# Optimization experiments

Measured on AMD Instinct MI355X. Metric: run time of the kernel, lower is better.

Reference implementation:

```python
import jax, jax.numpy as jnp
import numpy as np
import math

L, H, NH, DH, E, FF, A, I = 3, 1024, 8, 128, 768, 4096, 100, 50
B, S = 4, 1024
EPS = 1e-5


def _ln(x, g, b):
    m = jnp.mean(x, -1, keepdims=True)
    v = jnp.var(x, -1, keepdims=True)
    return (x - m) * jax.lax.rsqrt(v + EPS) * g + b


def _pos_encoding(seq, d):
    pos = jnp.arange(seq, dtype=jnp.float32)[:, None]
    div = jnp.exp(jnp.arange(0, d, 2, dtype=jnp.float32) * (-math.log(10000.0) / d))
    ang = pos * div  # [S, d/2]
    return jnp.stack([jnp.sin(ang), jnp.cos(ang)], axis=-1).reshape(seq, d)


def setup_inputs() -> dict:
    key = jax.random.key(0)
    ks = jax.random.split(key, 40)
    w = lambda k, s: jax.random.normal(k, s, jnp.float32) * 0.02
    z = lambda s: jnp.zeros(s, jnp.float32)
    d = {}
    d['frame_embeddings'] = jax.random.normal(ks[0], (B, S, E), jnp.float32)
    d['W_in'] = w(ks[1], (H, E)); d['b_in'] = z((H,))
    # _init_weights sets ALL 'weight' params (incl. LayerNorm) to normal(std=0.02)
    d['ln_in_g'] = w(ks[2], (H,)); d['ln_in_b'] = z((H,))
    d['qkv_w'] = w(ks[3], (L, 3 * H, H)); d['qkv_b'] = z((L, 3 * H))
    d['out_w'] = w(ks[4], (L, H, H)); d['out_b'] = z((L, H))
    d['ff1_w'] = w(ks[5], (L, FF, H)); d['ff1_b'] = z((L, FF))
    d['ff2_w'] = w(ks[6], (L, H, FF)); d['ff2_b'] = z((L, H))
    d['n1_g'] = w(ks[7], (L, H)); d['n1_b'] = z((L, H))
    d['n2_g'] = w(ks[8], (L, H)); d['n2_b'] = z((L, H))
    d['ln_out_g'] = w(ks[9], (H,)); d['ln_out_b'] = z((H,))
    d['a1_w'] = w(ks[10], (H, H)); d['a1_b'] = z((H,))
    d['a2_w'] = w(ks[11], (A, H)); d['a2_b'] = z((A,))
    d['i1_w'] = w(ks[12], (H, H)); d['i1_b'] = z((H,))
    d['i2_w'] = w(ks[13], (I, H)); d['i2_b'] = z((I,))
    d['c1_w'] = w(ks[14], (H // 2, H)); d['c1_b'] = z((H // 2,))
    d['c2_w'] = w(ks[15], (1, H // 2)); d['c2_b'] = z((1,))
    d['p_w'] = w(ks[16], (1, H)); d['p_b'] = z((1,))
    d['smoothing_factor'] = jnp.float32(0.7)
    return d


def _encoder_layer(x, qkv_w, qkv_b, out_w, out_b, ff1_w, ff1_b, ff2_w, ff2_b, n1_g, n1_b, n2_g, n2_b):
    # PyTorch post-norm TransformerEncoderLayer (eval: no dropout)
    b, s, _ = x.shape
    qkv = x @ qkv_w.T + qkv_b  # [B,S,3H]
    q, k, v = jnp.split(qkv, 3, axis=-1)
    q = q.reshape(b, s, NH, DH)
    k = k.reshape(b, s, NH, DH)
    v = v.reshape(b, s, NH, DH)
    scores = jnp.einsum('bqhd,bkhd->bhqk', q, k) / math.sqrt(DH)
    attn = jax.nn.softmax(scores, axis=-1)
    ctx = jnp.einsum('bhqk,bkhd->bqhd', attn, v).reshape(b, s, H)
    x = _ln(x + (ctx @ out_w.T + out_b), n1_g, n1_b)
    ff = jax.nn.gelu(x @ ff1_w.T + ff1_b, approximate=False) @ ff2_w.T + ff2_b
    return _ln(x + ff, n2_g, n2_b)


def reference(frame_embeddings, W_in, b_in, ln_in_g, ln_in_b, qkv_w, qkv_b, out_w, out_b,
              ff1_w, ff1_b, ff2_w, ff2_b, n1_g, n1_b, n2_g, n2_b, ln_out_g, ln_out_b,
              a1_w, a1_b, a2_w, a2_b, i1_w, i1_b, i2_w, i2_b, c1_w, c1_b, c2_w, c2_b,
              p_w, p_b, smoothing_factor):
    b, s, _ = frame_embeddings.shape
    h = frame_embeddings @ W_in.T + b_in
    h = h + _pos_encoding(s, H)[None]
    h = _ln(h, ln_in_g, ln_in_b)
    for l in range(L):
        h = _encoder_layer(h, qkv_w[l], qkv_b[l], out_w[l], out_b[l], ff1_w[l], ff1_b[l],
                           ff2_w[l], ff2_b[l], n1_g[l], n1_b[l], n2_g[l], n2_b[l])
    ctx = _ln(h, ln_out_g, ln_out_b)
    action = jax.nn.gelu(ctx @ a1_w.T + a1_b, approximate=False) @ a2_w.T + a2_b  # [B,S,A]
    instr = jax.nn.gelu(ctx @ i1_w.T + i1_b, approximate=False) @ i2_w.T + i2_b  # [B,S,I]
    conf = jax.nn.sigmoid(jax.nn.gelu(ctx @ c1_w.T + c1_b, approximate=False) @ c2_w.T + c2_b)
    # EMA smoothing over time as a single scan (replaces the per-step Python loop)
    sf = jnp.clip(smoothing_factor, 0.0, 1.0)
    both = jnp.concatenate([action, instr], axis=-1)  # [B,S,A+I]
    def step(carry, xt):
        sm = sf * xt + (1.0 - sf) * carry
        return sm, sm
    _, ys = jax.lax.scan(step, both[:, 0], jnp.swapaxes(both[:, 1:], 0, 1))
    smoothed = jnp.concatenate([both[:, :1], jnp.swapaxes(ys, 0, 1)], axis=1)
    action = smoothed[..., :A]
    instr = smoothed[..., A:]
    pool = jax.nn.softmax(ctx @ p_w.T + p_b, axis=1)  # [B,S,1]
    global_ctx = jnp.einsum('bsi,bsh->bih', pool, ctx)[:, 0]  # [B,H]
    return action, instr, conf, pool[..., 0], global_ctx
```

## Files before the change

kernel.cpp:

```cpp
#include <hip/hip_runtime.h>

typedef __attribute__((ext_vector_type(8))) short frag8;
typedef __attribute__((ext_vector_type(4))) float facc4;

#define MFMA16(a,b,c) __builtin_amdgcn_mfma_f32_16x16x32_bf16((a),(b),(c),0,0,0)

__device__ __forceinline__ unsigned short f2bf(float f){
  unsigned int u = __builtin_bit_cast(unsigned int, f);
  u += 0x7FFFu + ((u >> 16) & 1u);
  return (unsigned short)(u >> 16);
}
__device__ __forceinline__ float bf2f(unsigned short h){
  unsigned int u = ((unsigned int)h) << 16;
  return __builtin_bit_cast(float, u);
}
__device__ __forceinline__ float gelu_f(float x){
  return 0.5f * x * (1.0f + erff(x * 0.70710678118654752440f));
}
__device__ __forceinline__ void gload16(const void* g, void* l){
  __builtin_amdgcn_global_load_lds(
      (const __attribute__((address_space(1))) void*)g,
      (__attribute__((address_space(3))) void*)l, 16, 0, 0);
}

struct CvtSeg { const float* src; unsigned short* dst; long total; long blk_start; int rows_src; int K; };
struct CvtArgs { CvtSeg seg[12]; int nseg; };

__global__ void convert_all(CvtArgs a){
  long blk = blockIdx.x;
  int si = 0;
  for (int i = 1; i < a.nseg; i++) if (blk >= a.seg[i].blk_start) si = i;
  CvtSeg s = a.seg[si];
  long i = ((blk - s.blk_start) * 256 + threadIdx.x) * 4L;
  if (i >= s.total) return;
  long row = i / s.K;
  ushort4 o;
  if (row < s.rows_src){
    float4 v = *(const float4*)(s.src + i);
    o.x = f2bf(v.x); o.y = f2bf(v.y); o.z = f2bf(v.z); o.w = f2bf(v.w);
  } else { o.x = 0; o.y = 0; o.z = 0; o.w = 0; }
  *(ushort4*)(s.dst + i) = o;
}

__global__ void pe_kernel(float* __restrict__ pe){
  const int s = blockIdx.x;
  const int t = threadIdx.x;
  float4 o;
#pragma unroll
  for (int e = 0; e < 4; e++){
    int c = t * 4 + e;
    int i2 = c & ~1;
    float dv = expf(-0.0089944730195080f * (float)i2);
    float ang = (float)s * dv;
    ((float*)&o)[e] = (c & 1) ? cosf(ang) : sinf(ang);
  }
  *(float4*)(pe + (size_t)s * 1024 + t * 4) = o;
}

template<int KTOT, int EPI>
__global__ __launch_bounds__(256, 2)
void gemm_p4(const unsigned short* __restrict__ A,
             const unsigned short* __restrict__ W,
             const float* __restrict__ bias,
             void* __restrict__ Cout,
             int ldC, int coloff, int nvalid)
{
  constexpr int BK = 32;
  constexpr int NT = KTOT / BK;
  constexpr int SLOT = 16384;
  static_assert(NT >= 3, "pipeline needs >=3 K-steps");
  __shared__ char lds[4 * SLOT];

  const int tid = threadIdx.x;
  const int w = tid >> 6, lane = tid & 63;
  const int lh = lane & 15, lq = lane >> 4;
  const int wm = w >> 1, wn = w & 1;
  const long row0 = (long)blockIdx.x * 128;
  const long col0 = (long)blockIdx.y * 128;

  facc4 acc[4][4];
  const facc4 vz = {0.f, 0.f, 0.f, 0.f};
#pragma unroll
  for (int r = 0; r < 4; r++)
#pragma unroll
    for (int c = 0; c < 4; c++) acc[r][c] = vz;

  const unsigned short* srcs[4];
#pragma unroll
  for (int i = 0; i < 4; i++){
    const int f = i * 4 + w;
    srcs[i] = (f < 8)
      ? A + (row0 + f * 16 + lh) * (long)KTOT + lq * 8
      : W + (col0 + (f - 8) * 16 + lh) * (long)KTOT + lq * 8;
  }

  auto stage = [&](int slot, int k0){
#pragma unroll
    for (int i = 0; i < 4; i++)
      gload16(srcs[i] + k0, lds + slot * SLOT + (i * 4 + w) * 1024);
  };

  stage(0, 0);
  stage(1, BK);

  for (int t = 0; t < NT; t++){
    if (t + 2 < NT){
      stage((t + 2) & 3, (t + 2) * BK);
      asm volatile("s_waitcnt vmcnt(8)\ns_barrier" ::: "memory");
    } else if (t + 1 < NT){
      asm volatile("s_waitcnt vmcnt(4)\ns_barrier" ::: "memory");
    } else {
      asm volatile("s_waitcnt vmcnt(0)\ns_barrier" ::: "memory");
    }
    __builtin_amdgcn_sched_barrier(0);
    const char* base = lds + (t & 3) * SLOT;
    frag8 af[4], bf[4];
#pragma unroll
    for (int r = 0; r < 4; r++)
      af[r] = *(const frag8*)(base + (wm * 4 + r) * 1024 + lane * 16);
#pragma unroll
    for (int c = 0; c < 4; c++)
      bf[c] = *(const frag8*)(base + 8192 + (wn * 4 + c) * 1024 + lane * 16);
    __builtin_amdgcn_s_setprio(1);
#pragma unroll
    for (int r = 0; r < 4; r++)
#pragma unroll
      for (int c = 0; c < 4; c++)
        acc[r][c] = MFMA16(af[r], bf[c], acc[r][c]);
    __builtin_amdgcn_s_setprio(0);
  }

  if (EPI == 0){
#pragma unroll
    for (int c = 0; c < 4; c++){
      const long gcol = col0 + wn * 64 + c * 16 + lh;
      const bool ok = gcol < nvalid;
      const float bv = ok ? bias[gcol] : 0.f;
#pragma unroll
      for (int r = 0; r < 4; r++){
#pragma unroll
        for (int j = 0; j < 4; j++){
          if (!ok) continue;
          const long grow = row0 + wm * 64 + r * 16 + lq * 4 + j;
          ((float*)Cout)[grow * (long)ldC + coloff + gcol] = acc[r][c][j] + bv;
        }
      }
    }
  } else {
    __syncthreads();
    unsigned short* Es = (unsigned short*)lds;
#pragma unroll
    for (int c = 0; c < 4; c++){
      const int colt = wn * 64 + c * 16 + lh;
      const long gcol = col0 + colt;
      const float bv = (gcol < nvalid) ? bias[gcol] : 0.f;
#pragma unroll
      for (int r = 0; r < 4; r++){
#pragma unroll
        for (int j = 0; j < 4; j++){
          float v = acc[r][c][j] + bv;
          if (EPI == 2) v = gelu_f(v);
          Es[(wm * 64 + r * 16 + lq * 4 + j) * 128 + colt] = f2bf(v);
        }
      }
    }
    __syncthreads();
    unsigned short* outp = (unsigned short*)Cout;
#pragma unroll
    for (int it = 0; it < 8; it++){
      const int row = w * 32 + it * 4 + lq;
      const long grow = row0 + row;
      const long gc0 = col0 + lh * 8;
      const unsigned short* s = &Es[row * 128 + lh * 8];
      if (gc0 + 8 <= nvalid){
        *(uint4*)(outp + grow * (long)ldC + coloff + gc0) = *(const uint4*)s;
      } else {
#pragma unroll
        for (int e = 0; e < 8; e++)
          if (gc0 + e < nvalid) outp[grow * (long)ldC + coloff + gc0 + e] = s[e];
      }
    }
  }
}

__global__ __launch_bounds__(256)
void ln_kernel(const float* __restrict__ a, const float* __restrict__ bsrc, int bmode,
               const float* __restrict__ g, const float* __restrict__ be,
               float* __restrict__ of32, unsigned short* __restrict__ obf)
{
  const int row = blockIdx.x;
  const int t = threadIdx.x;
  float4 x = ((const float4*)(a + (size_t)row * 1024))[t];
  if (bmode){
    const size_t brow = (bmode == 1) ? (size_t)row : (size_t)(row & 1023);
    float4 y = ((const float4*)(bsrc + brow * 1024))[t];
    x.x += y.x; x.y += y.y; x.z += y.z; x.w += y.w;
  }
  float s = x.x + x.y + x.z + x.w;
  float ss = x.x * x.x + x.y * x.y + x.z * x.z + x.w * x.w;
#pragma unroll
  for (int mk = 1; mk < 64; mk <<= 1){ s += __shfl_xor(s, mk); ss += __shfl_xor(ss, mk); }
  __shared__ float red[8];
  const int w = t >> 6, lane = t & 63;
  if (lane == 0){ red[w] = s; red[4 + w] = ss; }
  __syncthreads();
  s = red[0] + red[1] + red[2] + red[3];
  ss = red[4] + red[5] + red[6] + red[7];
  const float mean = s * (1.f / 1024.f);
  const float var = ss * (1.f / 1024.f) - mean * mean;
  const float rstd = rsqrtf(var + 1e-5f);
  float4 gg = ((const float4*)g)[t];
  float4 bb = ((const float4*)be)[t];
  float4 o;
  o.x = (x.x - mean) * rstd * gg.x + bb.x;
  o.y = (x.y - mean) * rstd * gg.y + bb.y;
  o.z = (x.z - mean) * rstd * gg.z + bb.z;
  o.w = (x.w - mean) * rstd * gg.w + bb.w;
  if (of32) ((float4*)(of32 + (size_t)row * 1024))[t] = o;
  if (obf){
    ushort4 hh;
    hh.x = f2bf(o.x); hh.y = f2bf(o.y); hh.z = f2bf(o.z); hh.w = f2bf(o.w);
    ((ushort4*)(obf + (size_t)row * 1024))[t] = hh;
  }
}

__global__ void transpose_v(const unsigned short* __restrict__ qkv, unsigned short* __restrict__ vt){
  __shared__ unsigned short t[32][33];
  const int s0 = blockIdx.x * 32;
  const int d0 = blockIdx.y * 32;
  const int bh = blockIdx.z;
  const int b = bh >> 3, h = bh & 7;
  const int tx = threadIdx.x, ty = threadIdx.y;
#pragma unroll
  for (int j = 0; j < 4; j++){
    int srow = ty + j * 8;
    t[srow][tx] = qkv[(size_t)(b * 1024 + s0 + srow) * 3072 + 2048 + h * 128 + d0 + tx];
  }
  __syncthreads();
#pragma unroll
  for (int j = 0; j < 4; j++){
    int drow = ty + j * 8;
    vt[((size_t)bh * 128 + d0 + drow) * 1024 + s0 + tx] = t[tx][drow];
  }
}

__global__ __launch_bounds__(256, 2)
void attn_kernel(const unsigned short* __restrict__ qkv,
                 const unsigned short* __restrict__ vt,
                 unsigned short* __restrict__ ctx)
{
  const int qt = blockIdx.x, h = blockIdx.y, b = blockIdx.z;
  const int tid = threadIdx.x;
  const int w = tid >> 6, lane = tid & 63;
  const int lh = lane & 15, lq = lane >> 4;

  __shared__ unsigned short Ks[2][64 * 128];
  __shared__ unsigned short Vs[2][128 * 64];
  __shared__ unsigned short P[4][16][72];

  const float scale = 0.08838834764831845f;
  const int q0 = qt * 64 + w * 16;

  frag8 qf[4];
#pragma unroll
  for (int kk = 0; kk < 4; kk++)
    qf[kk] = *(const frag8*)(qkv + ((size_t)(b * 1024 + q0 + lh)) * 3072 + h * 128 + kk * 32 + lq * 8);

  const unsigned short* Kg = qkv + (size_t)b * 1024 * 3072 + 1024 + h * 128;
  const unsigned short* Vg = vt + (size_t)(b * 8 + h) * 128 * 1024;

  const int k_rsub = lane >> 4;
  const int k_c    = lane & 15;
  const int v_rsub = lane >> 3;
  const int v_c    = lane & 7;

  auto stage = [&](int buf, int kv0){
#pragma unroll
    for (int i = 0; i < 4; i++){
      const int seg = i * 4 + w;
      const int kr = seg * 4 + k_rsub;
      const int ksc = k_c ^ (kr & 7);
      gload16(Kg + (size_t)(kv0 + kr) * 3072 + ksc * 8,
              (char*)Ks + buf * 16384 + seg * 1024);
      const int vr = seg * 8 + v_rsub;
      const int vsc = v_c ^ (vr & 7);
      gload16(Vg + (size_t)vr * 1024 + kv0 + vsc * 8,
              (char*)Vs + buf * 16384 + seg * 1024);
    }
  };

  facc4 O[8];
  const facc4 vz = {0.f, 0.f, 0.f, 0.f};
#pragma unroll
  for (int c = 0; c < 8; c++) O[c] = vz;
  float m[4], l[4];
#pragma unroll
  for (int j = 0; j < 4; j++){ m[j] = -3.0e38f; l[j] = 0.f; }

  stage(0, 0);
  __syncthreads();

  for (int t = 0; t < 16; t++){
    const int cur = t & 1;
    if (t < 15) stage(cur ^ 1, (t + 1) * 64);

    facc4 S[4];
#pragma unroll
    for (int c = 0; c < 4; c++) S[c] = vz;
    const char* Kb = (const char*)Ks + cur * 16384;
#pragma unroll
    for (int c = 0; c < 4; c++){
      const int row = c * 16 + lh;
#pragma unroll
      for (int kk = 0; kk < 4; kk++){
        frag8 kf = *(const frag8*)(Kb + row * 256 + ((kk * 64 + lq * 16) ^ ((row & 7) << 4)));
        S[c] = MFMA16(qf[kk], kf, S[c]);
      }
    }
    float tmax[4] = {-3.0e38f, -3.0e38f, -3.0e38f, -3.0e38f};
#pragma unroll
    for (int c = 0; c < 4; c++)
#pragma unroll
      for (int j = 0; j < 4; j++){
        float v = S[c][j] * scale;
        S[c][j] = v;
        tmax[j] = fmaxf(tmax[j], v);
      }
#pragma unroll
    for (int mk = 1; mk < 16; mk <<= 1)
#pragma unroll
      for (int j = 0; j < 4; j++) tmax[j] = fmaxf(tmax[j], __shfl_xor(tmax[j], mk));
    float al[4], rs[4];
#pragma unroll
    for (int j = 0; j < 4; j++){
      float mn = fmaxf(m[j], tmax[j]);
      al[j] = __expf(m[j] - mn);
      m[j] = mn;
      rs[j] = 0.f;
    }
#pragma unroll
    for (int c = 0; c < 4; c++)
#pragma unroll
      for (int j = 0; j < 4; j++){
        float p = __expf(S[c][j] - m[j]);
        S[c][j] = p;
        rs[j] += p;
      }
#pragma unroll
    for (int mk = 1; mk < 16; mk <<= 1)
#pragma unroll
      for (int j = 0; j < 4; j++) rs[j] += __shfl_xor(rs[j], mk);
#pragma unroll
    for (int j = 0; j < 4; j++) l[j] = l[j] * al[j] + rs[j];
#pragma unroll
    for (int c = 0; c < 8; c++)
#pragma unroll
      for (int j = 0; j < 4; j++) O[c][j] *= al[j];

#pragma unroll
    for (int c = 0; c < 4; c++)
#pragma unroll
      for (int j = 0; j < 4; j++)
        P[w][lq * 4 + j][c * 16 + lh] = f2bf(S[c][j]);
    frag8 pf[2];
#pragma unroll
    for (int kk = 0; kk < 2; kk++)
      pf[kk] = *(const frag8*)&P[w][lh][kk * 32 + lq * 8];

    const char* Vb = (const char*)Vs + cur * 16384;
#pragma unroll
    for (int c2 = 0; c2 < 8; c2++){
      const int row = c2 * 16 + lh;
#pragma unroll
      for (int kk = 0; kk < 2; kk++){
        frag8 vf = *(const frag8*)(Vb + row * 128 + ((kk * 64 + lq * 16) ^ ((row & 7) << 4)));
        O[c2] = MFMA16(pf[kk], vf, O[c2]);
      }
    }
    __syncthreads();
  }

  unsigned short* Es = (unsigned short*)Ks;
#pragma unroll
  for (int c2 = 0; c2 < 8; c2++)
#pragma unroll
    for (int j = 0; j < 4; j++)
      Es[w * 2048 + (lq * 4 + j) * 128 + c2 * 16 + lh] = f2bf(O[c2][j] / l[j]);
  __syncthreads();
  const int token0 = b * 1024 + qt * 64 + w * 16;
#pragma unroll
  for (int rr = 0; rr < 16; rr++){
    const unsigned int val = *(const unsigned int*)&Es[w * 2048 + rr * 128 + lane * 2];
    *(unsigned int*)(ctx + (size_t)(token0 + rr) * 1024 + h * 128 + lane * 2) = val;
  }
}

__global__ void ema_kernel(const float* __restrict__ both, const float* __restrict__ sfp,
                           float* __restrict__ oact, float* __restrict__ oinst)
{
  const int idx = blockIdx.x * 256 + threadIdx.x;
  if (idx >= 4 * 1024 * 150) return;
  const int c = idx % 150;
  const int bs = idx / 150;
  const int s = bs & 1023;
  float sf = fminf(fmaxf(sfp[0], 0.f), 1.f);
  const float q = 1.f - sf;
  const float* p = both + (size_t)bs * 160 + c;
  float acc = 0.f, wgt = sf;
  const int klim = (s < 28) ? s : 28;
  for (int k = 0; k < klim; k++){ acc += wgt * p[-(long)k * 160]; wgt *= q; }
  if (s <= 28) acc += powf(q, (float)s) * p[-(long)s * 160];
  if (c < 100) oact[(size_t)bs * 100 + c] = acc;
  else         oinst[(size_t)bs * 50 + (c - 100)] = acc;
}

__global__ void head_c2(const unsigned short* __restrict__ x, const float* __restrict__ wv,
                        const float* __restrict__ bv, float* __restrict__ out)
{
  const int row = blockIdx.x * 4 + (threadIdx.x >> 6);
  const int lane = threadIdx.x & 63;
  float acc = 0.f;
#pragma unroll
  for (int i = 0; i < 8; i++){
    int cidx = i * 64 + lane;
    acc += bf2f(x[(size_t)row * 512 + cidx]) * wv[cidx];
  }
#pragma unroll
  for (int mk = 1; mk < 64; mk <<= 1) acc += __shfl_xor(acc, mk);
  if (lane == 0) out[row] = 1.f / (1.f + __expf(-(acc + bv[0])));
}

__global__ void head_p(const float* __restrict__ x, const float* __restrict__ wv,
                       const float* __restrict__ bv, float* __restrict__ out)
{
  const int row = blockIdx.x * 4 + (threadIdx.x >> 6);
  const int lane = threadIdx.x & 63;
  float acc = 0.f;
#pragma unroll
  for (int i = 0; i < 16; i++){
    int cidx = i * 64 + lane;
    acc += x[(size_t)row * 1024 + cidx] * wv[cidx];
  }
#pragma unroll
  for (int mk = 1; mk < 64; mk <<= 1) acc += __shfl_xor(acc, mk);
  if (lane == 0) out[row] = acc + bv[0];
}

__global__ void pool_softmax(const float* __restrict__ scores, float* __restrict__ poolws,
                             float* __restrict__ outpool)
{
  const int b = blockIdx.x, t = threadIdx.x;
  float4 v = ((const float4*)(scores + (size_t)b * 1024))[t];
  float mx = fmaxf(fmaxf(v.x, v.y), fmaxf(v.z, v.w));
#pragma unroll
  for (int mk = 1; mk < 64; mk <<= 1) mx = fmaxf(mx, __shfl_xor(mx, mk));
  __shared__ float red[8];
  const int w = t >> 6, lane = t & 63;
  if (lane == 0) red[w] = mx;
  __syncthreads();
  mx = fmaxf(fmaxf(red[0], red[1]), fmaxf(red[2], red[3]));
  float4 e;
  e.x = __expf(v.x - mx); e.y = __expf(v.y - mx); e.z = __expf(v.z - mx); e.w = __expf(v.w - mx);
  float sum = e.x + e.y + e.z + e.w;
#pragma unroll
  for (int mk = 1; mk < 64; mk <<= 1) sum += __shfl_xor(sum, mk);
  if (lane == 0) red[4 + w] = sum;
  __syncthreads();
  sum = red[4] + red[5] + red[6] + red[7];
  const float inv = 1.f / sum;
  e.x *= inv; e.y *= inv; e.z *= inv; e.w *= inv;
  ((float4*)(poolws + (size_t)b * 1024))[t] = e;
  ((float4*)(outpool + (size_t)b * 1024))[t] = e;
}

__global__ void globalctx_kernel(const float* __restrict__ pool, const float* __restrict__ ctxf,
                                 float* __restrict__ out)
{
  const int hh = blockIdx.x * 256 + threadIdx.x;
  const int b = blockIdx.y;
  const float* p = pool + (size_t)b * 1024;
  const float* c = ctxf + (size_t)b * 1024 * 1024 + hh;
  float acc = 0.f;
  for (int s = 0; s < 1024; s++) acc += p[s] * c[(size_t)s * 1024];
  out[(size_t)b * 1024 + hh] = acc;
}

extern "C" void kernel_launch(void* const* d_in, const int* in_sizes, int n_in,
                              void* d_out, int out_size, void* d_ws, size_t ws_size,
                              hipStream_t stream)
{
  if (n_in < 34) return;
  const float* emb     = (const float*)d_in[0];
  const float* W_in    = (const float*)d_in[1];
  const float* b_in    = (const float*)d_in[2];
  const float* ln_in_g = (const float*)d_in[3];
  const float* ln_in_b = (const float*)d_in[4];
  const float* qkv_w   = (const float*)d_in[5];
  const float* qkv_b   = (const float*)d_in[6];
  const float* out_w   = (const float*)d_in[7];
  const float* out_b   = (const float*)d_in[8];
  const float* ff1_w   = (const float*)d_in[9];
  const float* ff1_b   = (const float*)d_in[10];
  const float* ff2_w   = (const float*)d_in[11];
  const float* ff2_b   = (const float*)d_in[12];
  const float* n1_g    = (const float*)d_in[13];
  const float* n1_b    = (const float*)d_in[14];
  const float* n2_g    = (const float*)d_in[15];
  const float* n2_b    = (const float*)d_in[16];
  const float* ln_out_g= (const float*)d_in[17];
  const float* ln_out_b= (const float*)d_in[18];
  const float* a1_w    = (const float*)d_in[19];
  const float* a1_b    = (const float*)d_in[20];
  const float* a2_w    = (const float*)d_in[21];
  const float* a2_b    = (const float*)d_in[22];
  const float* i1_w    = (const float*)d_in[23];
  const float* i1_b    = (const float*)d_in[24];
  const float* i2_w    = (const float*)d_in[25];
  const float* i2_b    = (const float*)d_in[26];
  const float* c1_w    = (const float*)d_in[27];
  const float* c1_b    = (const float*)d_in[28];
  const float* c2_w    = (const float*)d_in[29];
  const float* c2_b    = (const float*)d_in[30];
  const float* p_w     = (const float*)d_in[31];
  const float* p_b     = (const float*)d_in[32];
  const float* sfp     = (const float*)d_in[33];

  char* ws = (char*)d_ws;
  size_t off = 0;
  auto alloc = [&](size_t bytes) -> void* {
    void* p = ws + off;
    off += (bytes + 255) & ~(size_t)255;
    return p;
  };
  unsigned short* emb_bf  = (unsigned short*)alloc((size_t)4096 * 768 * 2);
  unsigned short* Win_bf  = (unsigned short*)alloc((size_t)1024 * 768 * 2);
  unsigned short* qkvw_bf = (unsigned short*)alloc((size_t)3 * 3072 * 1024 * 2);
  unsigned short* outw_bf = (unsigned short*)alloc((size_t)3 * 1024 * 1024 * 2);
  unsigned short* ff1w_bf = (unsigned short*)alloc((size_t)3 * 4096 * 1024 * 2);
  unsigned short* ff2w_bf = (unsigned short*)alloc((size_t)3 * 1024 * 4096 * 2);
  unsigned short* a1w_bf  = (unsigned short*)alloc((size_t)1024 * 1024 * 2);
  unsigned short* a2w_bf  = (unsigned short*)alloc((size_t)128 * 1024 * 2);
  unsigned short* i1w_bf  = (unsigned short*)alloc((size_t)1024 * 1024 * 2);
  unsigned short* i2w_bf  = (unsigned short*)alloc((size_t)128 * 1024 * 2);
  unsigned short* c1w_bf  = (unsigned short*)alloc((size_t)512 * 1024 * 2);
  float* pe      = (float*)alloc((size_t)1024 * 1024 * 4);
  float* t0      = (float*)alloc((size_t)4096 * 1024 * 4);
  float* hres    = (float*)alloc((size_t)4096 * 1024 * 4);
  unsigned short* h_bf = (unsigned short*)alloc((size_t)4096 * 1024 * 2);
  unsigned short* buf1 = (unsigned short*)alloc((size_t)4096 * 4096 * 2);
  unsigned short* vtb  = (unsigned short*)alloc((size_t)4096 * 1024 * 2);
  unsigned short* ctxb = (unsigned short*)alloc((size_t)4096 * 1024 * 2);
  float* bothb  = (float*)alloc((size_t)4096 * 160 * 4);
  float* scores = (float*)alloc((size_t)4096 * 4);
  float* poolws = (float*)alloc((size_t)4096 * 4);
  if (off > ws_size) return;

  float* out_action = (float*)d_out;
  float* out_instr  = out_action + 4 * 1024 * 100;
  float* out_conf   = out_instr + 4 * 1024 * 50;
  float* out_pool   = out_conf + 4 * 1024;
  float* out_gctx   = out_pool + 4 * 1024;

  CvtArgs ca{};
  long blk = 0;
  auto addseg = [&](const float* src, unsigned short* dst, long rows_src, long rows_dst, long Kd){
    CvtSeg& sg = ca.seg[ca.nseg];
    sg.src = src; sg.dst = dst; sg.total = rows_dst * Kd;
    sg.rows_src = (int)rows_src; sg.K = (int)Kd; sg.blk_start = blk;
    blk += (sg.total + 1023) / 1024;
    ca.nseg++;
  };
  addseg(emb,   emb_bf,  4096, 4096, 768);
  addseg(W_in,  Win_bf,  1024, 1024, 768);
  addseg(qkv_w, qkvw_bf, 9216, 9216, 1024);
  addseg(out_w, outw_bf, 3072, 3072, 1024);
  addseg(ff1_w, ff1w_bf, 12288, 12288, 1024);
  addseg(ff2_w, ff2w_bf, 3072, 3072, 4096);
  addseg(a1_w,  a1w_bf,  1024, 1024, 1024);
  addseg(a2_w,  a2w_bf,  100,  128,  1024);
  addseg(i1_w,  i1w_bf,  1024, 1024, 1024);
  addseg(i2_w,  i2w_bf,  50,   128,  1024);
  addseg(c1_w,  c1w_bf,  512,  512,  1024);
  convert_all<<<dim3((unsigned)blk), dim3(256), 0, stream>>>(ca);

  pe_kernel<<<dim3(1024), dim3(256), 0, stream>>>(pe);

  gemm_p4<768,0><<<dim3(32, 8), dim3(256), 0, stream>>>(emb_bf, Win_bf, b_in, t0, 1024, 0, 1024);
  ln_kernel<<<dim3(4096), dim3(256), 0, stream>>>(t0, pe, 2, ln_in_g, ln_in_b, hres, h_bf);

  for (int l = 0; l < 3; l++){
    gemm_p4<1024,1><<<dim3(32, 24), dim3(256), 0, stream>>>(h_bf, qkvw_bf + (size_t)l * 3072 * 1024,
                                                       qkv_b + (size_t)l * 3072, buf1, 3072, 0, 3072);
    transpose_v<<<dim3(32, 4, 32), dim3(32, 8), 0, stream>>>(buf1, vtb);
    attn_kernel<<<dim3(16, 8, 4), dim3(256), 0, stream>>>(buf1, vtb, ctxb);
    gemm_p4<1024,0><<<dim3(32, 8), dim3(256), 0, stream>>>(ctxb, outw_bf + (size_t)l * 1024 * 1024,
                                                      out_b + (size_t)l * 1024, t0, 1024, 0, 1024);
    ln_kernel<<<dim3(4096), dim3(256), 0, stream>>>(hres, t0, 1, n1_g + l * 1024, n1_b + l * 1024, hres, h_bf);
    gemm_p4<1024,2><<<dim3(32, 32), dim3(256), 0, stream>>>(h_bf, ff1w_bf + (size_t)l * 4096 * 1024,
                                                       ff1_b + (size_t)l * 4096, buf1, 4096, 0, 4096);
    gemm_p4<4096,0><<<dim3(32, 8), dim3(256), 0, stream>>>(buf1, ff2w_bf + (size_t)l * 1024 * 4096,
                                                      ff2_b + (size_t)l * 1024, t0, 1024, 0, 1024);
    ln_kernel<<<dim3(4096), dim3(256), 0, stream>>>(hres, t0, 1, n2_g + l * 1024, n2_b + l * 1024, hres, h_bf);
  }

  ln_kernel<<<dim3(4096), dim3(256), 0, stream>>>(hres, nullptr, 0, ln_out_g, ln_out_b, t0, ctxb);

  gemm_p4<1024,2><<<dim3(32, 8), dim3(256), 0, stream>>>(ctxb, a1w_bf, a1_b, vtb, 1024, 0, 1024);
  gemm_p4<1024,0><<<dim3(32, 1), dim3(256), 0, stream>>>(vtb, a2w_bf, a2_b, bothb, 160, 0, 100);
  gemm_p4<1024,2><<<dim3(32, 8), dim3(256), 0, stream>>>(ctxb, i1w_bf, i1_b, vtb, 1024, 0, 1024);
  gemm_p4<1024,0><<<dim3(32, 1), dim3(256), 0, stream>>>(vtb, i2w_bf, i2_b, bothb, 160, 100, 50);
  gemm_p4<1024,2><<<dim3(32, 4), dim3(256), 0, stream>>>(ctxb, c1w_bf, c1_b, vtb, 512, 0, 512);
  head_c2<<<dim3(1024), dim3(256), 0, stream>>>(vtb, c2_w, c2_b, out_conf);
  head_p<<<dim3(1024), dim3(256), 0, stream>>>(t0, p_w, p_b, scores);
  pool_softmax<<<dim3(4), dim3(256), 0, stream>>>(scores, poolws, out_pool);
  globalctx_kernel<<<dim3(4, 4), dim3(256), 0, stream>>>(poolws, t0, out_gctx);
  ema_kernel<<<dim3(2400), dim3(256), 0, stream>>>(bothb, sfp, out_action, out_instr);
}
```

Baseline: 1.084 ms.

## Replace multi-stage pipelined GEMM with single-buffer BK=64 runtime-K GEMM

Swaps the 4-slot, three-deep pipelined GEMM (K as a template constant, BK=32) for a single-buffered kernel with BK=64 and runtime K. Each step loads the tile, syncs, runs two MFMA sub-steps and syncs again. This halves LDS usage and the number of K iterations, but drops the overlap of global loads with MFMA compute. The epilogue store mapping is also changed to coalesce by thread index.

After: 1.348 ms. 24.4% more time.

```diff
diff --git a/kernel.cpp b/kernel.cpp
--- a/kernel.cpp
+++ b/kernel.cpp
@@ -57,20 +57,15 @@
   *(float4*)(pe + (size_t)s * 1024 + t * 4) = o;
 }
 
-template<int KTOT, int EPI>
+template<int EPI>
 __global__ __launch_bounds__(256, 2)
-void gemm_p4(const unsigned short* __restrict__ A,
+void gemm_v9(const unsigned short* __restrict__ A,
              const unsigned short* __restrict__ W,
              const float* __restrict__ bias,
              void* __restrict__ Cout,
-             int ldC, int coloff, int nvalid)
-{
-  constexpr int BK = 32;
-  constexpr int NT = KTOT / BK;
-  constexpr int SLOT = 16384;
-  static_assert(NT >= 3, "pipeline needs >=3 K-steps");
-  __shared__ char lds[4 * SLOT];
-
+             int K, int ldC, int coloff, int nvalid)
+{
+  __shared__ char lds[32768];
   const int tid = threadIdx.x;
   const int w = tid >> 6, lane = tid & 63;
   const int lh = lane & 15, lq = lane >> 4;
@@ -85,49 +80,41 @@
 #pragma unroll
     for (int c = 0; c < 4; c++) acc[r][c] = vz;
 
-  const unsigned short* srcs[4];
-#pragma unroll
-  for (int i = 0; i < 4; i++){
-    const int f = i * 4 + w;
-    srcs[i] = (f < 8)
-      ? A + (row0 + f * 16 + lh) * (long)KTOT + lq * 8
-      : W + (col0 + (f - 8) * 16 + lh) * (long)KTOT + lq * 8;
-  }
-
-  auto stage = [&](int slot, int k0){
-#pragma unroll
-    for (int i = 0; i < 4; i++)
-      gload16(srcs[i] + k0, lds + slot * SLOT + (i * 4 + w) * 1024);
-  };
-
-  stage(0, 0);
-  stage(1, BK);
-
-  for (int t = 0; t < NT; t++){
-    if (t + 2 < NT){
-      stage((t + 2) & 3, (t + 2) * BK);
-      asm volatile("s_waitcnt vmcnt(8)\ns_barrier" ::: "memory");
-    } else if (t + 1 < NT){
-      asm volatile("s_waitcnt vmcnt(4)\ns_barrier" ::: "memory");
+  const unsigned short* srcs[8];
+#pragma unroll
+  for (int j = 0; j < 8; j++){
+    const int f = j * 4 + w;
+    if (f < 16){
+      const int rf = f >> 1, kf = f & 1;
+      srcs[j] = A + (row0 + rf * 16 + lh) * (long)K + kf * 32 + lq * 8;
     } else {
-      asm volatile("s_waitcnt vmcnt(0)\ns_barrier" ::: "memory");
-    }
-    __builtin_amdgcn_sched_barrier(0);
-    const char* base = lds + (t & 3) * SLOT;
-    frag8 af[4], bf[4];
-#pragma unroll
-    for (int r = 0; r < 4; r++)
-      af[r] = *(const frag8*)(base + (wm * 4 + r) * 1024 + lane * 16);
-#pragma unroll
-    for (int c = 0; c < 4; c++)
-      bf[c] = *(const frag8*)(base + 8192 + (wn * 4 + c) * 1024 + lane * 16);
-    __builtin_amdgcn_s_setprio(1);
-#pragma unroll
-    for (int r = 0; r < 4; r++)
+      const int g = f - 16;
+      const int cf = g >> 1, kf = g & 1;
+      srcs[j] = W + (col0 + cf * 16 + lh) * (long)K + kf * 32 + lq * 8;
+    }
+  }
+
+  for (int k0 = 0; k0 < K; k0 += 64){
+#pragma unroll
+    for (int j = 0; j < 8; j++)
+      gload16(srcs[j] + k0, lds + (j * 4 + w) * 1024);
+    __syncthreads();
+#pragma unroll
+    for (int ks = 0; ks < 2; ks++){
+      frag8 af[4], bf[4];
+#pragma unroll
+      for (int r = 0; r < 4; r++)
+        af[r] = *(const frag8*)(lds + (((wm * 4 + r) << 1) + ks) * 1024 + lane * 16);
 #pragma unroll
       for (int c = 0; c < 4; c++)
-        acc[r][c] = MFMA16(af[r], bf[c], acc[r][c]);
-    __builtin_amdgcn_s_setprio(0);
+        bf[c] = *(const frag8*)(lds + 16384 + (((wn * 4 + c) << 1) + ks) * 1024 + lane * 16);
+#pragma unroll
+      for (int r = 0; r < 4; r++)
+#pragma unroll
+        for (int c = 0; c < 4; c++)
+          acc[r][c] = MFMA16(af[r], bf[c], acc[r][c]);
+    }
+    __syncthreads();
   }
 
   if (EPI == 0){
@@ -147,7 +134,6 @@
       }
     }
   } else {
-    __syncthreads();
     unsigned short* Es = (unsigned short*)lds;
 #pragma unroll
     for (int c = 0; c < 4; c++){
@@ -168,10 +154,11 @@
     unsigned short* outp = (unsigned short*)Cout;
 #pragma unroll
     for (int it = 0; it < 8; it++){
-      const int row = w * 32 + it * 4 + lq;
+      const int chunk = tid + it * 256;
+      const int row = chunk >> 4, cb = chunk & 15;
+      const long gc0 = col0 + cb * 8;
+      const unsigned short* s = &Es[row * 128 + cb * 8];
       const long grow = row0 + row;
-      const long gc0 = col0 + lh * 8;
-      const unsigned short* s = &Es[row * 128 + lh * 8];
       if (gc0 + 8 <= nvalid){
         *(uint4*)(outp + grow * (long)ldC + coloff + gc0) = *(const uint4*)s;
       } else {
@@ -585,31 +572,31 @@
 
   pe_kernel<<<dim3(1024), dim3(256), 0, stream>>>(pe);
 
-  gemm_p4<768,0><<<dim3(32, 8), dim3(256), 0, stream>>>(emb_bf, Win_bf, b_in, t0, 1024, 0, 1024);
+  gemm_v9<0><<<dim3(32, 8), dim3(256), 0, stream>>>(emb_bf, Win_bf, b_in, t0, 768, 1024, 0, 1024);
   ln_kernel<<<dim3(4096), dim3(256), 0, stream>>>(t0, pe, 2, ln_in_g, ln_in_b, hres, h_bf);
 
   for (int l = 0; l < 3; l++){
-    gemm_p4<1024,1><<<dim3(32, 24), dim3(256), 0, stream>>>(h_bf, qkvw_bf + (size_t)l * 3072 * 1024,
-                                                       qkv_b + (size_t)l * 3072, buf1, 3072, 0, 3072);
+    gemm_v9<1><<<dim3(32, 24), dim3(256), 0, stream>>>(h_bf, qkvw_bf + (size_t)l * 3072 * 1024,
+                                                       qkv_b + (size_t)l * 3072, buf1, 1024, 3072, 0, 3072);
     transpose_v<<<dim3(32, 4, 32), dim3(32, 8), 0, stream>>>(buf1, vtb);
     attn_kernel<<<dim3(16, 8, 4), dim3(256), 0, stream>>>(buf1, vtb, ctxb);
-    gemm_p4<1024,0><<<dim3(32, 8), dim3(256), 0, stream>>>(ctxb, outw_bf + (size_t)l * 1024 * 1024,
-                                                      out_b + (size_t)l * 1024, t0, 1024, 0, 1024);
+    gemm_v9<0><<<dim3(32, 8), dim3(256), 0, stream>>>(ctxb, outw_bf + (size_t)l * 1024 * 1024,
+                                                      out_b + (size_t)l * 1024, t0, 1024, 1024, 0, 1024);
     ln_kernel<<<dim3(4096), dim3(256), 0, stream>>>(hres, t0, 1, n1_g + l * 1024, n1_b + l * 1024, hres, h_bf);
-    gemm_p4<1024,2><<<dim3(32, 32), dim3(256), 0, stream>>>(h_bf, ff1w_bf + (size_t)l * 4096 * 1024,
-                                                       ff1_b + (size_t)l * 4096, buf1, 4096, 0, 4096);
-    gemm_p4<4096,0><<<dim3(32, 8), dim3(256), 0, stream>>>(buf1, ff2w_bf + (size_t)l * 1024 * 4096,
-                                                      ff2_b + (size_t)l * 1024, t0, 1024, 0, 1024);
+    gemm_v9<2><<<dim3(32, 32), dim3(256), 0, stream>>>(h_bf, ff1w_bf + (size_t)l * 4096 * 1024,
+                                                       ff1_b + (size_t)l * 4096, buf1, 1024, 4096, 0, 4096);
+    gemm_v9<0><<<dim3(32, 8), dim3(256), 0, stream>>>(buf1, ff2w_bf + (size_t)l * 1024 * 4096,
+                                                      ff2_b + (size_t)l * 1024, t0, 4096, 1024, 0, 1024);
     ln_kernel<<<dim3(4096), dim3(256), 0, stream>>>(hres, t0, 1, n2_g + l * 1024, n2_b + l * 1024, hres, h_bf);
   }
 
   ln_kernel<<<dim3(4096), dim3(256), 0, stream>>>(hres, nullptr, 0, ln_out_g, ln_out_b, t0, ctxb);
 
-  gemm_p4<1024,2><<<dim3(32, 8), dim3(256), 0, stream>>>(ctxb, a1w_bf, a1_b, vtb, 1024, 0, 1024);
-  gemm_p4<1024,0><<<dim3(32, 1), dim3(256), 0, stream>>>(vtb, a2w_bf, a2_b, bothb, 160, 0, 100);
-  gemm_p4<1024,2><<<dim3(32, 8), dim3(256), 0, stream>>>(ctxb, i1w_bf, i1_b, vtb, 1024, 0, 1024);
-  gemm_p4<1024,0><<<dim3(32, 1), dim3(256), 0, stream>>>(vtb, i2w_bf, i2_b, bothb, 160, 100, 50);
-  gemm_p4<1024,2><<<dim3(32, 4), dim3(256), 0, stream>>>(ctxb, c1w_bf, c1_b, vtb, 512, 0, 512);
+  gemm_v9<2><<<dim3(32, 8), dim3(256), 0, stream>>>(ctxb, a1w_bf, a1_b, vtb, 1024, 1024, 0, 1024);
+  gemm_v9<0><<<dim3(32, 1), dim3(256), 0, stream>>>(vtb, a2w_bf, a2_b, bothb, 1024, 160, 0, 100);
+  gemm_v9<2><<<dim3(32, 8), dim3(256), 0, stream>>>(ctxb, i1w_bf, i1_b, vtb, 1024, 1024, 0, 1024);
+  gemm_v9<0><<<dim3(32, 1), dim3(256), 0, stream>>>(vtb, i2w_bf, i2_b, bothb, 1024, 160, 100, 50);
+  gemm_v9<2><<<dim3(32, 4), dim3(256), 0, stream>>>(ctxb, c1w_bf, c1_b, vtb, 1024, 512, 0, 512);
   head_c2<<<dim3(1024), dim3(256), 0, stream>>>(vtb, c2_w, c2_b, out_conf);
   head_p<<<dim3(1024), dim3(256), 0, stream>>>(t0, p_w, p_b, scores);
   pool_softmax<<<dim3(4), dim3(256), 0, stream>>>(scores, poolws, out_pool);
```
